# Kernel optimization log

Measured on AMD Instinct MI355X. Metric: run time of the kernel, lower is better.

The kernel has to match this reference:

```python
import jax, jax.numpy as jnp
import numpy as np

EMBED_DIM = 256; N_HEADS = 8; HEAD_DIM = 32; N_PAIRS = 16
POS_DIM = 2; N_LEVELS = 4; NBH = [3, 5, 7, 9]
N_Q = 2048; BATCH = 2; FULL = 128
SPATIAL_THETA = 100.0; LEVEL_THETA = 10.0
LN_EPS = 1e-5


def _grids():
    offs, lvls = [], []
    for l, s in enumerate(NBH):
        ax = np.arange(s)
        g = np.stack(np.meshgrid(ax, ax, indexing='ij'), -1).reshape(-1, 2)
        offs.append(g - (s - 1) // 2)
        lvls.append(np.full(s * s, l))
    return (np.concatenate(offs).astype(np.int32), np.concatenate(lvls).astype(np.int32))

OFFSETS, LEVEL_IDS = _grids()  # [164,2], [164]
K_PER_Q = OFFSETS.shape[0]


def _apply_rope(x, pos, freqs):
    # x: [..., n_heads, n_pairs, 2]; pos: [..., 3]; freqs: [3, n_pairs]
    ang = pos @ freqs                      # [..., n_pairs]
    c = jnp.cos(ang)[..., None, :]         # broadcast over heads
    s = jnp.sin(ang)[..., None, :]
    x1, x2 = x[..., 0], x[..., 1]
    return jnp.stack([x1 * c - x2 * s, x1 * s + x2 * c], axis=-1)


def setup_inputs() -> dict:
    key = jax.random.key(0)
    ks = jax.random.split(key, 8)
    scale = EMBED_DIM ** -0.5
    i = jnp.arange(N_PAIRS, dtype=jnp.float32) / N_PAIRS
    rope_freqs = jnp.stack([SPATIAL_THETA ** -i, SPATIAL_THETA ** -i, LEVEL_THETA ** -i])  # [3,16]
    level_spatial_shapes = jnp.array([[FULL >> l, FULL >> l] for l in range(N_LEVELS)], jnp.int32)
    return {
        'query': jax.random.normal(ks[0], (N_Q, EMBED_DIM), jnp.float32),
        'query_spatial_positions': jax.random.uniform(ks[1], (N_Q, POS_DIM), jnp.float32) * (FULL - 1),
        'stacked_feature_maps': jax.random.normal(ks[2], (BATCH, N_LEVELS, FULL, FULL, EMBED_DIM), jnp.float32) * 0.02,
        'norm_w': jnp.ones((EMBED_DIM,), jnp.float32),
        'norm_b': jnp.zeros((EMBED_DIM,), jnp.float32),
        'q_w': jax.random.normal(ks[3], (EMBED_DIM, EMBED_DIM), jnp.float32) * scale,
        'k_w': jax.random.normal(ks[4], (EMBED_DIM, EMBED_DIM), jnp.float32) * scale,
        'v_w': jax.random.normal(ks[5], (EMBED_DIM, EMBED_DIM), jnp.float32) * scale,
        'out_w': jax.random.normal(ks[6], (EMBED_DIM, EMBED_DIM), jnp.float32) * scale,
        'rope_freqs': rope_freqs,
        'query_batch_offsets': jnp.array([0, N_Q // 2, N_Q], jnp.int32),
        'level_spatial_shapes': level_spatial_shapes,
    }


def reference(query, query_spatial_positions, stacked_feature_maps, norm_w, norm_b,
              q_w, k_w, v_w, out_w, rope_freqs, query_batch_offsets, level_spatial_shapes):
    n_q = query.shape[0]
    residual = query

    # pre-LayerNorm
    mu = query.mean(-1, keepdims=True)
    var = query.var(-1, keepdims=True)
    x = (query - mu) * jax.lax.rsqrt(var + LN_EPS) * norm_w + norm_b

    # query projection + RoPE (spatial dims + level dim; queries sit at max-res level 0)
    q = x @ q_w
    qpos = jnp.concatenate([query_spatial_positions, jnp.zeros((n_q, 1), query.dtype)], -1)  # [n_q,3]
    q_rot = _apply_rope(q.reshape(n_q, N_HEADS, N_PAIRS, 2), qpos, rope_freqs).reshape(n_q, N_HEADS, HEAD_DIM)

    # multilevel neighborhood indices
    shapes_f = level_spatial_shapes.astype(query.dtype)               # [L,2]
    scaling = shapes_f / shapes_f.max(0)                              # [L,2]
    scaled = query_spatial_positions[:, None, :] * scaling[None]      # [n_q,L,2]
    centers = jnp.floor(scaled).astype(jnp.int32)                     # [n_q,L,2]
    lvl = jnp.asarray(LEVEL_IDS)                                      # [K]
    idx = centers[:, lvl, :] + jnp.asarray(OFFSETS)[None]             # [n_q,K,2]
    lsh = level_spatial_shapes[lvl]                                   # [K,2]
    valid = jnp.all((idx >= 0) & (idx < lsh[None]), -1)               # [n_q,K]
    idxc = jnp.clip(idx, 0, lsh[None] - 1)

    # per-query batch ids from offsets
    b = jnp.searchsorted(query_batch_offsets, jnp.arange(n_q, dtype=query_batch_offsets.dtype), side='right') - 1

    # sparse gather of key/value features (unspecified -> zero)
    feats = stacked_feature_maps[b[:, None], lvl[None, :], idxc[..., 0], idxc[..., 1]]  # [n_q,K,E]
    feats = feats * valid[..., None].astype(feats.dtype)

    k = feats @ k_w
    v = feats @ v_w

    # key positions at full scale + level coordinate
    stride = (shapes_f.max(0)[None] / shapes_f)[lvl]                  # [K,2]
    kpos_sp = (idx.astype(query.dtype) + 0.5) * stride[None]          # [n_q,K,2]
    kpos = jnp.concatenate([kpos_sp, jnp.broadcast_to(lvl.astype(query.dtype), (n_q, K_PER_Q))[..., None]], -1)
    k_rot = _apply_rope(k.reshape(n_q, K_PER_Q, N_HEADS, N_PAIRS, 2), kpos, rope_freqs)
    k_rot = k_rot.reshape(n_q, K_PER_Q, N_HEADS, HEAD_DIM)

    # attention over the 164 gathered keys per query
    logits = jnp.einsum('nhd,nkhd->nhk', q_rot, k_rot) / np.sqrt(HEAD_DIM)
    logits = jnp.where(valid[:, None, :], logits, jnp.asarray(-1e9, logits.dtype))
    attn = jax.nn.softmax(logits, axis=-1)
    out = jnp.einsum('nhk,nkhd->nhd', attn, v.reshape(n_q, K_PER_Q, N_HEADS, HEAD_DIM))
    out = out.reshape(n_q, EMBED_DIM) @ out_w
    return out + residual
```

## Files before the change

### kernel.cpp

```cpp
#include <hip/hip_runtime.h>
#include <hip/hip_bf16.h>

typedef unsigned short u16;
typedef short short8 __attribute__((ext_vector_type(8)));
typedef float f32x4 __attribute__((ext_vector_type(4)));

#define ROWS_PER_BATCH 21760
#define TOT_ROWS 43520

__device__ __forceinline__ u16 f2bf(float f){
  unsigned u = __builtin_bit_cast(unsigned, f);
  u += 0x7FFFu + ((u >> 16) & 1u);
  return (u16)(u >> 16);
}
__device__ __forceinline__ float bf2f(u16 h){
  return __builtin_bit_cast(float, ((unsigned)h) << 16);
}
__device__ __forceinline__ float bflo(unsigned u){ return __builtin_bit_cast(float, u << 16); }
__device__ __forceinline__ float bfhi(unsigned u){ return __builtin_bit_cast(float, u & 0xFFFF0000u); }
__device__ __forceinline__ unsigned pk2bf(float a, float b){
  __hip_bfloat162 h = __float22bfloat162_rn(make_float2(a, b));
  union { __hip_bfloat162 h2; unsigned u; } cv; cv.h2 = h; return cv.u;
}

__global__ __launch_bounds__(256) void prep_kernel(
    const float* __restrict__ qw, const float* __restrict__ kw,
    const float* __restrict__ vw, const float* __restrict__ ow,
    const float* __restrict__ q, const float* __restrict__ nw,
    const float* __restrict__ nb,
    u16* __restrict__ wtq, u16* __restrict__ wtk,
    u16* __restrict__ wtv, u16* __restrict__ wto, u16* __restrict__ x){
  const int bx = blockIdx.x;
  const int t = threadIdx.x;
  if (bx < 128){
    int e = bx * 256 + t;
    int which = e >> 13;
    int r = e & 8191;
    int cg = r >> 9;
    int kk = (r >> 6) & 7;
    int lane = r & 63;
    int quad = lane >> 4, mn = lane & 15;
    const float* s = which == 0 ? qw : which == 1 ? kw : which == 2 ? vw : ow;
    u16* d       = which == 0 ? wtq : which == 1 ? wtk : which == 2 ? wtv : wto;
    const float* base = s + (kk * 32 + quad * 8) * 256 + cg * 16 + mn;
    float e8[8];
    #pragma unroll
    for (int j = 0; j < 8; ++j) e8[j] = base[j * 256];
    uint4 o = { pk2bf(e8[0], e8[1]), pk2bf(e8[2], e8[3]),
                pk2bf(e8[4], e8[5]), pk2bf(e8[6], e8[7]) };
    *(uint4*)(d + (size_t)r * 8) = o;
  } else {
    const int row = (bx - 128) * 4 + (t >> 6);
    const int lane = t & 63;
    const float4 v = *(const float4*)(q + (size_t)row * 256 + lane * 4);
    float s1 = v.x + v.y + v.z + v.w;
    float s2 = v.x*v.x + v.y*v.y + v.z*v.z + v.w*v.w;
    #pragma unroll
    for (int o = 32; o > 0; o >>= 1){
      s1 += __shfl_xor(s1, o);
      s2 += __shfl_xor(s2, o);
    }
    float mu = s1 * (1.0f / 256.0f);
    float var = s2 * (1.0f / 256.0f) - mu * mu;
    float rs = rsqrtf(var + 1e-5f);
    const float4 wv = *(const float4*)(nw + lane * 4);
    const float4 bv = *(const float4*)(nb + lane * 4);
    float o0 = (v.x - mu) * rs * wv.x + bv.x;
    float o1 = (v.y - mu) * rs * wv.y + bv.y;
    float o2 = (v.z - mu) * rs * wv.z + bv.z;
    float o3 = (v.w - mu) * rs * wv.w + bv.w;
    uint2 pk = { pk2bf(o0, o1), pk2bf(o2, o3) };
    *(uint2*)(x + (size_t)row * 256 + lane * 4) = pk;
  }
}

__global__ __launch_bounds__(64, 4) void kv_gemm(const float* __restrict__ fm,
        const u16* __restrict__ wtkp, const u16* __restrict__ wtvp,
        const float* __restrict__ rope,
        u16* __restrict__ krot, u16* __restrict__ vmap){
  __shared__ float slab[16][66];
  __shared__ unsigned sh_cs[16][16];

  const int lane = threadIdx.x;
  const int row0 = blockIdx.x * 16;

  const int b = row0 / ROWS_PER_BATCH;
  const int rr = row0 - b * ROWS_PER_BATCH;
  int l, loff;
  if (rr < 16384)      { l = 0; loff = 0; }
  else if (rr < 20480) { l = 1; loff = 16384; }
  else if (rr < 21504) { l = 2; loff = 20480; }
  else                 { l = 3; loff = 21504; }
  const int logW = 7 - l;
  const int Wm1 = (128 >> l) - 1;
  const int cell0 = rr - loff;
  const float* fmbase = fm + (size_t)(b * 4 + l) * (128 * 128 * 256);

  const int mn = lane & 15;
  const int quad = lane >> 4;

  short8 af[8];
  {
    int cell = cell0 + mn;
    int y = cell >> logW, x = cell & Wm1;
    const float* arow = fmbase + (((y << 7) + x) << 8) + quad * 8;
    #pragma unroll
    for (int kk = 0; kk < 8; ++kk){
      float4 a0 = *(const float4*)(arow + kk * 32);
      float4 a1 = *(const float4*)(arow + kk * 32 + 4);
      union { short8 s; uint4 u; } cv;
      cv.u = (uint4){ pk2bf(a0.x, a0.y), pk2bf(a0.z, a0.w),
                      pk2bf(a1.x, a1.y), pk2bf(a1.z, a1.w) };
      af[kk] = cv.s;
    }
  }

  #pragma unroll
  for (int i = 0; i < 4; ++i){
    int id = i * 64 + lane;
    int lr = id >> 4, p = id & 15;
    int cell = cell0 + lr;
    int i0 = cell >> logW;
    int i1 = cell & Wm1;
    float fs = (float)(1 << l);
    float kx = ((float)i0 + 0.5f) * fs;
    float ky = ((float)i1 + 0.5f) * fs;
    float ang = kx * rope[p] + ky * rope[16 + p] + (float)l * rope[32 + p];
    sh_cs[lr][p] = pk2bf(__cosf(ang), __sinf(ang));
  }

  for (int m = 0; m < 2; ++m){
    const u16* wtp = m ? wtvp : wtkp;
    u16* outp = m ? vmap : krot;
    for (int cs2 = 0; cs2 < 4; ++cs2){
      const u16* wb = wtp + (size_t)((cs2 * 4 * 8) * 64 + lane) * 8;
      short8 bc[4], bn[4];
      #pragma unroll
      for (int tl = 0; tl < 4; ++tl)
        bc[tl] = *(const short8*)(wb + (size_t)(tl * 8) * 64 * 8);
      f32x4 acc[4];
      #pragma unroll
      for (int i = 0; i < 4; ++i) acc[i] = (f32x4){0.f, 0.f, 0.f, 0.f};
      #pragma unroll
      for (int kk = 0; kk < 8; ++kk){
        if (kk < 7){
          #pragma unroll
          for (int tl = 0; tl < 4; ++tl)
            bn[tl] = *(const short8*)(wb + (size_t)(tl * 8 + kk + 1) * 64 * 8);
        }
        #pragma unroll
        for (int tl = 0; tl < 4; ++tl)
          acc[tl] = __builtin_amdgcn_mfma_f32_16x16x32_bf16(af[kk], bc[tl], acc[tl], 0, 0, 0);
        #pragma unroll
        for (int tl = 0; tl < 4; ++tl) bc[tl] = bn[tl];
      }
      #pragma unroll
      for (int tl = 0; tl < 4; ++tl)
        #pragma unroll
        for (int r = 0; r < 4; ++r)
          slab[quad * 4 + r][tl * 16 + mn] = acc[tl][r];
      #pragma unroll
      for (int i = 0; i < 8; ++i){
        int pi = i * 64 + lane;
        int row = pi >> 5;
        int pl = pi & 31;
        float2 kv2 = *(const float2*)&slab[row][pl * 2];
        unsigned o;
        if (m == 0){
          unsigned csn = sh_cs[row][pl & 15];
          float c = bflo(csn), s = bfhi(csn);
          o = pk2bf(kv2.x * c - kv2.y * s, kv2.x * s + kv2.y * c);
        } else {
          o = pk2bf(kv2.x, kv2.y);
        }
        *(unsigned*)(outp + (size_t)(row0 + row) * 256 + cs2 * 64 + pl * 2) = o;
      }
    }
  }
}

__global__ __launch_bounds__(256) void gemm_xw(const u16* __restrict__ A,
        const u16* __restrict__ wt, const float* __restrict__ resid,
        float* __restrict__ out){
  const int t = threadIdx.x;
  const int row0 = blockIdx.x * 16;
  const int wv = t >> 6;
  const int lane = t & 63;
  const int mn = lane & 15;
  const int quad = lane >> 4;
  const int cg = blockIdx.y * 4 + wv;

  short8 af[8];
  {
    const u16* arow = A + (size_t)(row0 + mn) * 256 + quad * 8;
    #pragma unroll
    for (int kk = 0; kk < 8; ++kk)
      af[kk] = *(const short8*)(arow + kk * 32);
  }
  const u16* wb = wt + (size_t)((cg * 8) * 64 + lane) * 8;
  short8 bc = *(const short8*)wb;
  f32x4 acc = (f32x4){0.f, 0.f, 0.f, 0.f};
  #pragma unroll
  for (int kk = 0; kk < 8; ++kk){
    short8 bn;
    if (kk < 7) bn = *(const short8*)(wb + (size_t)(kk + 1) * 64 * 8);
    acc = __builtin_amdgcn_mfma_f32_16x16x32_bf16(af[kk], bc, acc, 0, 0, 0);
    bc = bn;
  }
  const int col = cg * 16 + mn;
  #pragma unroll
  for (int r = 0; r < 4; ++r){
    int row = row0 + quad * 4 + r;
    float val = acc[r];
    if (resid) val += resid[(size_t)row * 256 + col];
    out[(size_t)row * 256 + col] = val;
  }
}

__global__ __launch_bounds__(256) void attn3(
    const float* __restrict__ qraw, const float* __restrict__ qsp,
    const float* __restrict__ rope, const int* __restrict__ qbo, int nbo,
    const u16* __restrict__ krot, const u16* __restrict__ vmap,
    u16* __restrict__ ao){
  __shared__ float sh_q[4][8][33];
  __shared__ float sh_lg[4][168][8];
  __shared__ int   sh_row[4][168];
  __shared__ float sh_inv[4][8];
  const int t = threadIdx.x;
  const int w = t >> 6;
  const int lane = t & 63;
  const int qi = blockIdx.x * 4 + w;

  int bidx = 0;
  for (int j = 1; j < nbo; ++j) if (qi >= qbo[j]) bidx = j;
  const float p0 = qsp[qi * 2 + 0];
  const float p1 = qsp[qi * 2 + 1];

  #pragma unroll
  for (int it = 0; it < 4; ++it){
    int d = it * 64 + lane;
    float qv = qraw[(size_t)qi * 256 + d];
    int p = (d & 31) >> 1;
    float ang = p0 * rope[p] + p1 * rope[16 + p];
    float c = __cosf(ang), s = __sinf(ang);
    float partner = __shfl_xor(qv, 1);
    float val = (d & 1) ? (partner * s + qv * c) : (qv * c - partner * s);
    sh_q[w][d >> 5][d & 31] = val * 0.17677669529663687f;
  }

  #pragma unroll
  for (int it = 0; it < 3; ++it){
    int kk = it * 64 + lane;
    if (kk < 164){
      int l, dy, dx, loff;
      if (kk < 9)       { l = 0; int j = kk;      dy = j / 3 - 1; dx = j % 3 - 1; loff = 0; }
      else if (kk < 34) { l = 1; int j = kk - 9;  dy = j / 5 - 2; dx = j % 5 - 2; loff = 16384; }
      else if (kk < 83) { l = 2; int j = kk - 34; dy = j / 7 - 3; dx = j % 7 - 3; loff = 20480; }
      else              { l = 3; int j = kk - 83; dy = j / 9 - 4; dx = j % 9 - 4; loff = 21504; }
      float sc = 1.0f / (float)(1 << l);
      int i0 = (int)floorf(p0 * sc) + dy;
      int i1 = (int)floorf(p1 * sc) + dx;
      int W = 128 >> l;
      sh_row[w][kk] = (i0 < 0 || i0 >= W || i1 < 0 || i1 >= W)
                ? -1 : bidx * ROWS_PER_BATCH + loff + (i0 << (7 - l)) + i1;
    }
  }

  const int h = lane & 7;
  const int ksub = lane >> 3;
  float qreg[32];
  #pragma unroll
  for (int j = 0; j < 32; ++j) qreg[j] = sh_q[w][h][j];
  for (int pass = 0; pass < 21; ++pass){
    int kk = pass * 8 + ksub;
    if (kk < 164){
      int row = sh_row[w][kk];
      float lg = -1e9f;
      if (row >= 0){
        const uint4* kp = (const uint4*)(krot + (size_t)row * 256 + h * 32);
        uint4 A0 = kp[0], A1 = kp[1], A2 = kp[2], A3 = kp[3];
        unsigned uu[16];
        uu[0]=A0.x; uu[1]=A0.y; uu[2]=A0.z; uu[3]=A0.w;
        uu[4]=A1.x; uu[5]=A1.y; uu[6]=A1.z; uu[7]=A1.w;
        uu[8]=A2.x; uu[9]=A2.y; uu[10]=A2.z; uu[11]=A2.w;
        uu[12]=A3.x; uu[13]=A3.y; uu[14]=A3.z; uu[15]=A3.w;
        lg = 0.f;
        #pragma unroll
        for (int j = 0; j < 16; ++j)
          lg += qreg[2*j] * bflo(uu[j]) + qreg[2*j+1] * bfhi(uu[j]);
      }
      sh_lg[w][kk][h] = lg;
    }
  }

  float mx = -1e30f;
  for (int kk = ksub; kk < 164; kk += 8) mx = fmaxf(mx, sh_lg[w][kk][h]);
  #pragma unroll
  for (int o = 8; o < 64; o <<= 1) mx = fmaxf(mx, __shfl_xor(mx, o));
  float ssum = 0.f;
  for (int kk = ksub; kk < 164; kk += 8){
    float e = __expf(sh_lg[w][kk][h] - mx);
    sh_lg[w][kk][h] = e;
    ssum += e;
  }
  #pragma unroll
  for (int o = 8; o < 64; o <<= 1) ssum += __shfl_xor(ssum, o);
  if (ksub == 0) sh_inv[w][h] = 1.0f / ssum;

  const int hh = lane >> 3;
  float a0 = 0.f, a1 = 0.f, a2 = 0.f, a3 = 0.f;
  #pragma unroll 4
  for (int kk = 0; kk < 164; ++kk){
    int row = sh_row[w][kk];
    int rc = row < 0 ? 0 : row;
    uint2 vv = *(const uint2*)(vmap + (size_t)rc * 256 + lane * 4);
    float e = sh_lg[w][kk][hh];
    a0 += e * bflo(vv.x);
    a1 += e * bfhi(vv.x);
    a2 += e * bflo(vv.y);
    a3 += e * bfhi(vv.y);
  }
  float inv = sh_inv[w][hh];
  uint2 o = { pk2bf(a0 * inv, a1 * inv), pk2bf(a2 * inv, a3 * inv) };
  *(uint2*)(ao + (size_t)qi * 256 + lane * 4) = o;
}

extern "C" void kernel_launch(void* const* d_in, const int* in_sizes, int n_in,
                              void* d_out, int out_size, void* d_ws, size_t ws_size,
                              hipStream_t stream) {
  (void)n_in; (void)out_size; (void)ws_size;
  const float* query  = (const float*)d_in[0];
  const float* qsp    = (const float*)d_in[1];
  const float* fm     = (const float*)d_in[2];
  const float* norm_w = (const float*)d_in[3];
  const float* norm_b = (const float*)d_in[4];
  const float* q_w    = (const float*)d_in[5];
  const float* k_w    = (const float*)d_in[6];
  const float* v_w    = (const float*)d_in[7];
  const float* out_w  = (const float*)d_in[8];
  const float* rope   = (const float*)d_in[9];
  const int*   qbo    = (const int*)d_in[10];
  float* out = (float*)d_out;
  const int n_q = in_sizes[0] / 256;
  const int nbo = in_sizes[10];

  char* p = (char*)d_ws;
  u16* krot = (u16*)p;                       p += (size_t)TOT_ROWS * 256 * 2;
  u16* vmap = (u16*)p;                       p += (size_t)TOT_ROWS * 256 * 2;
  float* qraw = (float*)p;                   p += (size_t)n_q * 256 * 4;
  u16* xbf = (u16*)p;                        p += (size_t)n_q * 256 * 2;
  u16* wtq = (u16*)p;                        p += 65536 * 2;
  u16* wtk = (u16*)p;                        p += 65536 * 2;
  u16* wtv = (u16*)p;                        p += 65536 * 2;
  u16* wto = (u16*)p;
  u16* ao = xbf;

  hipLaunchKernelGGL(prep_kernel, dim3(128 + n_q / 4), dim3(256), 0, stream,
                     q_w, k_w, v_w, out_w, query, norm_w, norm_b,
                     wtq, wtk, wtv, wto, xbf);
  hipLaunchKernelGGL(kv_gemm, dim3(TOT_ROWS / 16), dim3(64), 0, stream,
                     fm, wtk, wtv, rope, krot, vmap);
  hipLaunchKernelGGL(gemm_xw, dim3(n_q / 16, 4), dim3(256), 0, stream,
                     xbf, wtq, (const float*)nullptr, qraw);
  hipLaunchKernelGGL(attn3, dim3(n_q / 4), dim3(256), 0, stream,
                     qraw, qsp, rope, qbo, nbo, krot, vmap, ao);
  hipLaunchKernelGGL(gemm_xw, dim3(n_q / 16, 4), dim3(256), 0, stream,
                     ao, wto, query, out);
}
```

Baseline: 272.6 us.

## Split each query's attention across four waves with block-level softmax reduction

The attention kernel now assigns one query per 256-thread block instead of one query per wave. Each of the four waves handles 41 of the 164 gathered keys, keeps its logits in registers, and then combines max, sum and partial PV results through shared memory and barriers. The V pass uses 16-byte loads covering half a row per lane. This is meant to give the gather latency more parallelism and launch four times as many blocks. In exchange it adds __syncthreads barriers and a cross-wave reduction.

```diff
diff --git a/kernel.cpp b/kernel.cpp
--- a/kernel.cpp
+++ b/kernel.cpp
@@ -217,112 +217,149 @@
   }
 }
 
-__global__ __launch_bounds__(256) void attn3(
+__global__ __launch_bounds__(256, 4) void attn3(
     const float* __restrict__ qraw, const float* __restrict__ qsp,
     const float* __restrict__ rope, const int* __restrict__ qbo, int nbo,
     const u16* __restrict__ krot, const u16* __restrict__ vmap,
     u16* __restrict__ ao){
-  __shared__ float sh_q[4][8][33];
-  __shared__ float sh_lg[4][168][8];
-  __shared__ int   sh_row[4][168];
-  __shared__ float sh_inv[4][8];
+  __shared__ float sh_q[8][33];
+  __shared__ int   sh_row[168];
+  __shared__ float sh_lg[168][8];
+  __shared__ float sh_wmax[4][8];
+  __shared__ float sh_psum[4][8];
+  __shared__ float sh_pv[4][256];
+
   const int t = threadIdx.x;
   const int w = t >> 6;
   const int lane = t & 63;
-  const int qi = blockIdx.x * 4 + w;
+  const int qi = blockIdx.x;
 
   int bidx = 0;
   for (int j = 1; j < nbo; ++j) if (qi >= qbo[j]) bidx = j;
   const float p0 = qsp[qi * 2 + 0];
   const float p1 = qsp[qi * 2 + 1];
 
-  #pragma unroll
-  for (int it = 0; it < 4; ++it){
-    int d = it * 64 + lane;
+  {
+    int d = t;
     float qv = qraw[(size_t)qi * 256 + d];
     int p = (d & 31) >> 1;
     float ang = p0 * rope[p] + p1 * rope[16 + p];
     float c = __cosf(ang), s = __sinf(ang);
     float partner = __shfl_xor(qv, 1);
     float val = (d & 1) ? (partner * s + qv * c) : (qv * c - partner * s);
-    sh_q[w][d >> 5][d & 31] = val * 0.17677669529663687f;
-  }
-
-  #pragma unroll
-  for (int it = 0; it < 3; ++it){
-    int kk = it * 64 + lane;
-    if (kk < 164){
-      int l, dy, dx, loff;
-      if (kk < 9)       { l = 0; int j = kk;      dy = j / 3 - 1; dx = j % 3 - 1; loff = 0; }
-      else if (kk < 34) { l = 1; int j = kk - 9;  dy = j / 5 - 2; dx = j % 5 - 2; loff = 16384; }
-      else if (kk < 83) { l = 2; int j = kk - 34; dy = j / 7 - 3; dx = j % 7 - 3; loff = 20480; }
-      else              { l = 3; int j = kk - 83; dy = j / 9 - 4; dx = j % 9 - 4; loff = 21504; }
-      float sc = 1.0f / (float)(1 << l);
-      int i0 = (int)floorf(p0 * sc) + dy;
-      int i1 = (int)floorf(p1 * sc) + dx;
-      int W = 128 >> l;
-      sh_row[w][kk] = (i0 < 0 || i0 >= W || i1 < 0 || i1 >= W)
-                ? -1 : bidx * ROWS_PER_BATCH + loff + (i0 << (7 - l)) + i1;
-    }
-  }
+    sh_q[d >> 5][d & 31] = val * 0.17677669529663687f;
+  }
+
+  if (t < 164){
+    int kk = t;
+    int l, dy, dx, loff;
+    if (kk < 9)       { l = 0; int j = kk;      dy = j / 3 - 1; dx = j % 3 - 1; loff = 0; }
+    else if (kk < 34) { l = 1; int j = kk - 9;  dy = j / 5 - 2; dx = j % 5 - 2; loff = 16384; }
+    else if (kk < 83) { l = 2; int j = kk - 34; dy = j / 7 - 3; dx = j % 7 - 3; loff = 20480; }
+    else              { l = 3; int j = kk - 83; dy = j / 9 - 4; dx = j % 9 - 4; loff = 21504; }
+    float sc = 1.0f / (float)(1 << l);
+    int i0 = (int)floorf(p0 * sc) + dy;
+    int i1 = (int)floorf(p1 * sc) + dx;
+    int W = 128 >> l;
+    sh_row[kk] = (i0 < 0 || i0 >= W || i1 < 0 || i1 >= W)
+              ? -1 : bidx * ROWS_PER_BATCH + loff + (i0 << (7 - l)) + i1;
+  }
+  __syncthreads();
 
   const int h = lane & 7;
   const int ksub = lane >> 3;
+  const int kbase = w * 41;
+
   float qreg[32];
   #pragma unroll
-  for (int j = 0; j < 32; ++j) qreg[j] = sh_q[w][h][j];
-  for (int pass = 0; pass < 21; ++pass){
-    int kk = pass * 8 + ksub;
-    if (kk < 164){
-      int row = sh_row[w][kk];
-      float lg = -1e9f;
-      if (row >= 0){
-        const uint4* kp = (const uint4*)(krot + (size_t)row * 256 + h * 32);
-        uint4 A0 = kp[0], A1 = kp[1], A2 = kp[2], A3 = kp[3];
-        unsigned uu[16];
-        uu[0]=A0.x; uu[1]=A0.y; uu[2]=A0.z; uu[3]=A0.w;
-        uu[4]=A1.x; uu[5]=A1.y; uu[6]=A1.z; uu[7]=A1.w;
-        uu[8]=A2.x; uu[9]=A2.y; uu[10]=A2.z; uu[11]=A2.w;
-        uu[12]=A3.x; uu[13]=A3.y; uu[14]=A3.z; uu[15]=A3.w;
-        lg = 0.f;
-        #pragma unroll
-        for (int j = 0; j < 16; ++j)
-          lg += qreg[2*j] * bflo(uu[j]) + qreg[2*j+1] * bfhi(uu[j]);
-      }
-      sh_lg[w][kk][h] = lg;
+  for (int j = 0; j < 32; ++j) qreg[j] = sh_q[h][j];
+
+  int rown[6];
+  #pragma unroll
+  for (int p = 0; p < 6; ++p){
+    int i = p * 8 + ksub;
+    rown[p] = (i < 41) ? sh_row[kbase + i] : -1;
+  }
+
+  float lgr[6];
+  #pragma unroll
+  for (int p = 0; p < 6; ++p){
+    float lg = -1e9f;
+    int row = rown[p];
+    if (row >= 0){
+      const uint4* kp = (const uint4*)(krot + (size_t)row * 256 + h * 32);
+      uint4 A0 = kp[0], A1 = kp[1], A2 = kp[2], A3 = kp[3];
+      unsigned uu[16];
+      uu[0]=A0.x; uu[1]=A0.y; uu[2]=A0.z; uu[3]=A0.w;
+      uu[4]=A1.x; uu[5]=A1.y; uu[6]=A1.z; uu[7]=A1.w;
+      uu[8]=A2.x; uu[9]=A2.y; uu[10]=A2.z; uu[11]=A2.w;
+      uu[12]=A3.x; uu[13]=A3.y; uu[14]=A3.z; uu[15]=A3.w;
+      lg = 0.f;
+      #pragma unroll
+      for (int j = 0; j < 16; ++j)
+        lg += qreg[2*j] * bflo(uu[j]) + qreg[2*j+1] * bfhi(uu[j]);
     }
-  }
-
-  float mx = -1e30f;
-  for (int kk = ksub; kk < 164; kk += 8) mx = fmaxf(mx, sh_lg[w][kk][h]);
+    lgr[p] = lg;
+  }
+
+  float mx = fmaxf(fmaxf(fmaxf(lgr[0], lgr[1]), fmaxf(lgr[2], lgr[3])),
+                   fmaxf(lgr[4], lgr[5]));
   #pragma unroll
   for (int o = 8; o < 64; o <<= 1) mx = fmaxf(mx, __shfl_xor(mx, o));
+  if (ksub == 0) sh_wmax[w][h] = mx;
+  __syncthreads();
+
+  const float gmx = fmaxf(fmaxf(sh_wmax[0][h], sh_wmax[1][h]),
+                          fmaxf(sh_wmax[2][h], sh_wmax[3][h]));
   float ssum = 0.f;
-  for (int kk = ksub; kk < 164; kk += 8){
-    float e = __expf(sh_lg[w][kk][h] - mx);
-    sh_lg[w][kk][h] = e;
-    ssum += e;
+  #pragma unroll
+  for (int p = 0; p < 6; ++p){
+    int i = p * 8 + ksub;
+    if (i < 41){
+      float e = __expf(lgr[p] - gmx);
+      sh_lg[kbase + i][h] = e;
+      ssum += e;
+    }
   }
   #pragma unroll
   for (int o = 8; o < 64; o <<= 1) ssum += __shfl_xor(ssum, o);
-  if (ksub == 0) sh_inv[w][h] = 1.0f / ssum;
-
-  const int hh = lane >> 3;
-  float a0 = 0.f, a1 = 0.f, a2 = 0.f, a3 = 0.f;
-  #pragma unroll 4
-  for (int kk = 0; kk < 164; ++kk){
-    int row = sh_row[w][kk];
+  if (ksub == 0) sh_psum[w][h] = ssum;
+  __syncthreads();
+
+  const int c = lane & 31;
+  const int p2 = lane >> 5;
+  const int hh = c >> 2;
+  const float invd = 1.0f / (sh_psum[0][hh] + sh_psum[1][hh] +
+                             sh_psum[2][hh] + sh_psum[3][hh]);
+  float a[8] = {0.f, 0.f, 0.f, 0.f, 0.f, 0.f, 0.f, 0.f};
+  #pragma unroll
+  for (int ii = 0; ii < 21; ++ii){
+    int i = ii * 2 + p2;
+    bool vld = i < 41;
+    int kk = kbase + (vld ? i : 0);
+    float e = vld ? sh_lg[kk][hh] : 0.f;
+    int row = vld ? sh_row[kk] : -1;
     int rc = row < 0 ? 0 : row;
-    uint2 vv = *(const uint2*)(vmap + (size_t)rc * 256 + lane * 4);
-    float e = sh_lg[w][kk][hh];
-    a0 += e * bflo(vv.x);
-    a1 += e * bfhi(vv.x);
-    a2 += e * bflo(vv.y);
-    a3 += e * bfhi(vv.y);
-  }
-  float inv = sh_inv[w][hh];
-  uint2 o = { pk2bf(a0 * inv, a1 * inv), pk2bf(a2 * inv, a3 * inv) };
-  *(uint2*)(ao + (size_t)qi * 256 + lane * 4) = o;
+    uint4 vv = *(const uint4*)(vmap + (size_t)rc * 256 + c * 8);
+    a[0] += e * bflo(vv.x); a[1] += e * bfhi(vv.x);
+    a[2] += e * bflo(vv.y); a[3] += e * bfhi(vv.y);
+    a[4] += e * bflo(vv.z); a[5] += e * bfhi(vv.z);
+    a[6] += e * bflo(vv.w); a[7] += e * bfhi(vv.w);
+  }
+  #pragma unroll
+  for (int j = 0; j < 8; ++j) a[j] += __shfl_xor(a[j], 32);
+  if (p2 == 0){
+    #pragma unroll
+    for (int j = 0; j < 8; ++j) sh_pv[w][c * 8 + j] = a[j] * invd;
+  }
+  __syncthreads();
+
+  if (t < 128){
+    int d0 = t * 2;
+    float s0 = sh_pv[0][d0]     + sh_pv[1][d0]     + sh_pv[2][d0]     + sh_pv[3][d0];
+    float s1 = sh_pv[0][d0 + 1] + sh_pv[1][d0 + 1] + sh_pv[2][d0 + 1] + sh_pv[3][d0 + 1];
+    *(unsigned*)(ao + (size_t)qi * 256 + d0) = pk2bf(s0, s1);
+  }
 }
 
 extern "C" void kernel_launch(void* const* d_in, const int* in_sizes, int n_in,
@@ -362,7 +399,7 @@
                      fm, wtk, wtv, rope, krot, vmap);
   hipLaunchKernelGGL(gemm_xw, dim3(n_q / 16, 4), dim3(256), 0, stream,
                      xbf, wtq, (const float*)nullptr, qraw);
-  hipLaunchKernelGGL(attn3, dim3(n_q / 4), dim3(256), 0, stream,
+  hipLaunchKernelGGL(attn3, dim3(n_q), dim3(256), 0, stream,
                      qraw, qsp, rope, qbo, nbo, krot, vmap, ao);
   hipLaunchKernelGGL(gemm_xw, dim3(n_q / 16, 4), dim3(256), 0, stream,
                      ao, wto, query, out);
```

Result: slower. 291.5 us (+6.9%).

## Process 32 rows per kv_gemm block to reuse weight fragments across two tiles

Applied to the files above, without the earlier changes.

Each kv_gemm wavefront now handles 32 feature rows (two 16-row MFMA tiles) instead of 16, so each loaded weight fragment feeds two MFMAs. The weight loads are restructured into a rolling 8-deep prefetch ring over 32 steps, and accumulators are flushed to shared memory per 16-column tile. This halves weight traffic per row and the block count, at the cost of more registers (launch bounds lowered to 2) and fewer blocks in flight. Level boundaries stay aligned because every level's row count is a multiple of 32.

```diff
diff --git a/kernel.cpp b/kernel.cpp
--- a/kernel.cpp
+++ b/kernel.cpp
@@ -74,15 +74,15 @@
   }
 }
 
-__global__ __launch_bounds__(64, 4) void kv_gemm(const float* __restrict__ fm,
+__global__ __launch_bounds__(64, 2) void kv_gemm(const float* __restrict__ fm,
         const u16* __restrict__ wtkp, const u16* __restrict__ wtvp,
         const float* __restrict__ rope,
         u16* __restrict__ krot, u16* __restrict__ vmap){
-  __shared__ float slab[16][66];
-  __shared__ unsigned sh_cs[16][16];
+  __shared__ float slab[32][66];
+  __shared__ unsigned sh_cs[32][16];
 
   const int lane = threadIdx.x;
-  const int row0 = blockIdx.x * 16;
+  const int row0 = blockIdx.x * 32;
 
   const int b = row0 / ROWS_PER_BATCH;
   const int rr = row0 - b * ROWS_PER_BATCH;
@@ -99,9 +99,10 @@
   const int mn = lane & 15;
   const int quad = lane >> 4;
 
-  short8 af[8];
-  {
-    int cell = cell0 + mn;
+  short8 af[2][8];
+  #pragma unroll
+  for (int g = 0; g < 2; ++g){
+    int cell = cell0 + g * 16 + mn;
     int y = cell >> logW, x = cell & Wm1;
     const float* arow = fmbase + (((y << 7) + x) << 8) + quad * 8;
     #pragma unroll
@@ -111,12 +112,12 @@
       union { short8 s; uint4 u; } cv;
       cv.u = (uint4){ pk2bf(a0.x, a0.y), pk2bf(a0.z, a0.w),
                       pk2bf(a1.x, a1.y), pk2bf(a1.z, a1.w) };
-      af[kk] = cv.s;
-    }
-  }
-
-  #pragma unroll
-  for (int i = 0; i < 4; ++i){
+      af[g][kk] = cv.s;
+    }
+  }
+
+  #pragma unroll
+  for (int i = 0; i < 8; ++i){
     int id = i * 64 + lane;
     int lr = id >> 4, p = id & 15;
     int cell = cell0 + lr;
@@ -133,34 +134,34 @@
     const u16* wtp = m ? wtvp : wtkp;
     u16* outp = m ? vmap : krot;
     for (int cs2 = 0; cs2 < 4; ++cs2){
-      const u16* wb = wtp + (size_t)((cs2 * 4 * 8) * 64 + lane) * 8;
-      short8 bc[4], bn[4];
+      const u16* wb = wtp + (size_t)((cs2 * 32) * 64 + lane) * 8;
+      short8 bq[8];
       #pragma unroll
-      for (int tl = 0; tl < 4; ++tl)
-        bc[tl] = *(const short8*)(wb + (size_t)(tl * 8) * 64 * 8);
-      f32x4 acc[4];
+      for (int j = 0; j < 8; ++j)
+        bq[j] = *(const short8*)(wb + (size_t)j * 512);
+      f32x4 acc0 = (f32x4){0.f, 0.f, 0.f, 0.f};
+      f32x4 acc1 = (f32x4){0.f, 0.f, 0.f, 0.f};
       #pragma unroll
-      for (int i = 0; i < 4; ++i) acc[i] = (f32x4){0.f, 0.f, 0.f, 0.f};
-      #pragma unroll
-      for (int kk = 0; kk < 8; ++kk){
-        if (kk < 7){
+      for (int j = 0; j < 32; ++j){
+        short8 bcur = bq[j & 7];
+        if (j + 8 < 32)
+          bq[j & 7] = *(const short8*)(wb + (size_t)(j + 8) * 512);
+        const int kk = j & 7;
+        acc0 = __builtin_amdgcn_mfma_f32_16x16x32_bf16(af[0][kk], bcur, acc0, 0, 0, 0);
+        acc1 = __builtin_amdgcn_mfma_f32_16x16x32_bf16(af[1][kk], bcur, acc1, 0, 0, 0);
+        if (kk == 7){
+          const int tl = j >> 3;
           #pragma unroll
-          for (int tl = 0; tl < 4; ++tl)
-            bn[tl] = *(const short8*)(wb + (size_t)(tl * 8 + kk + 1) * 64 * 8);
+          for (int r = 0; r < 4; ++r){
+            slab[quad * 4 + r][tl * 16 + mn]      = acc0[r];
+            slab[16 + quad * 4 + r][tl * 16 + mn] = acc1[r];
+          }
+          acc0 = (f32x4){0.f, 0.f, 0.f, 0.f};
+          acc1 = (f32x4){0.f, 0.f, 0.f, 0.f};
         }
-        #pragma unroll
-        for (int tl = 0; tl < 4; ++tl)
-          acc[tl] = __builtin_amdgcn_mfma_f32_16x16x32_bf16(af[kk], bc[tl], acc[tl], 0, 0, 0);
-        #pragma unroll
-        for (int tl = 0; tl < 4; ++tl) bc[tl] = bn[tl];
       }
       #pragma unroll
-      for (int tl = 0; tl < 4; ++tl)
-        #pragma unroll
-        for (int r = 0; r < 4; ++r)
-          slab[quad * 4 + r][tl * 16 + mn] = acc[tl][r];
-      #pragma unroll
-      for (int i = 0; i < 8; ++i){
+      for (int i = 0; i < 16; ++i){
         int pi = i * 64 + lane;
         int row = pi >> 5;
         int pl = pi & 31;
@@ -358,7 +359,7 @@
   hipLaunchKernelGGL(prep_kernel, dim3(128 + n_q / 4), dim3(256), 0, stream,
                      q_w, k_w, v_w, out_w, query, norm_w, norm_b,
                      wtq, wtk, wtv, wto, xbf);
-  hipLaunchKernelGGL(kv_gemm, dim3(TOT_ROWS / 16), dim3(64), 0, stream,
+  hipLaunchKernelGGL(kv_gemm, dim3(TOT_ROWS / 32), dim3(64), 0, stream,
                      fm, wtk, wtv, rope, krot, vmap);
   hipLaunchKernelGGL(gemm_xw, dim3(n_q / 16, 4), dim3(256), 0, stream,
                      xbf, wtq, (const float*)nullptr, qraw);
```

After: 290.0 us. 1.06x slower.
